# Kernel optimization log

Measured on AMD Instinct MI355X. Metric: run time of the kernel, lower is better.

## Reference

```python
import jax, jax.numpy as jnp
import numpy as np

N_HEADS = 16
D_EMB = 1024
D_HEAD = D_EMB // N_HEADS


def setup_inputs() -> dict:
    key = jax.random.key(0)
    ks = jax.random.split(key, 5)
    scale = 1.0 / np.sqrt(D_EMB)
    x = jax.random.normal(ks[0], (4, 2048, D_EMB), dtype=jnp.float32)
    W_in = jax.random.normal(ks[1], (3 * D_EMB, D_EMB), dtype=jnp.float32) * scale
    b_in = jax.random.normal(ks[2], (3 * D_EMB,), dtype=jnp.float32) * 0.01
    W_out = jax.random.normal(ks[3], (D_EMB, D_EMB), dtype=jnp.float32) * scale
    b_out = jax.random.normal(ks[4], (D_EMB,), dtype=jnp.float32) * 0.01
    return {"x": x, "W_in": W_in, "b_in": b_in, "W_out": W_out, "b_out": b_out}


def reference(x, W_in, b_in, W_out, b_out):
    b, s, d = x.shape
    qkv = x @ W_in.T + b_in  # [b, s, 3d]
    q, k, v = jnp.split(qkv, 3, axis=-1)
    def heads(t):
        return t.reshape(b, s, N_HEADS, D_HEAD).transpose(0, 2, 1, 3)  # [b,h,s,dh]
    q, k, v = heads(q), heads(k), heads(v)
    scores = jnp.einsum('bhqd,bhkd->bhqk', q, k)
    causal = jnp.tril(jnp.ones((s, s), dtype=bool))  # keep lower-triangular incl diag
    scores = jnp.where(causal, scores, -jnp.inf)
    scores = scores / np.sqrt(D_HEAD).astype(np.float32)
    w = jax.nn.softmax(scores, axis=-1)
    out = jnp.einsum('bhqk,bhkd->bhqd', w, v)  # [b,h,s,dh]
    out = out.transpose(0, 2, 1, 3).reshape(b, s, d)
    return out @ W_out.T + b_out
```

## Files before the change

kernel.cpp:

```cpp
#include <hip/hip_runtime.h>
#include <hip/hip_bf16.h>
#include <cstdint>


typedef float  floatx4  __attribute__((ext_vector_type(4)));
typedef __bf16 bf16x8   __attribute__((ext_vector_type(8)));
typedef __bf16 bf16x4   __attribute__((ext_vector_type(4)));
typedef short  shortx4  __attribute__((ext_vector_type(4)));
typedef unsigned int   uint32x2 __attribute__((ext_vector_type(2)));
typedef unsigned short ushortx8 __attribute__((ext_vector_type(8)));

#define MFMA16(a,b,c) __builtin_amdgcn_mfma_f32_16x16x32_bf16(a, b, c, 0, 0, 0)

__device__ __forceinline__ floatx4 mfma_k16(bf16x4 a, bf16x4 b, floatx4 c) {
#if defined(__HIP_DEVICE_COMPILE__)
#if __has_builtin(__builtin_amdgcn_mfma_f32_16x16x16_bf16)
  return __builtin_amdgcn_mfma_f32_16x16x16_bf16(a, b, c, 0, 0, 0);
#elif __has_builtin(__builtin_amdgcn_mfma_f32_16x16x16bf16_1k)
  return __builtin_amdgcn_mfma_f32_16x16x16bf16_1k(
      __builtin_bit_cast(shortx4, a), __builtin_bit_cast(shortx4, b), c, 0, 0, 0);
#else
  floatx4 d;
  asm("v_mfma_f32_16x16x16_bf16 %0, %1, %2, %3"
      : "=v"(d)
      : "v"(__builtin_bit_cast(uint32x2, a)),
        "v"(__builtin_bit_cast(uint32x2, b)), "v"(c));
  return d;
#endif
#else
  (void)a; (void)b;
  return c;
#endif
}

#define C_SCALE 0.18033688011112042f
#define M_STATIC 16.0f

__device__ __forceinline__ void gload_lds16(const void* g, void* l) {
  __builtin_amdgcn_global_load_lds(
      (__attribute__((address_space(1))) void*)(g),
      (__attribute__((address_space(3))) void*)(l), 16, 0, 0);
}

#define N_X4    2097152
#define N_WIN4  786432
#define N_WOUT4 262144
#define N_B4    768
__global__ __launch_bounds__(256) void cast_fused(
    const float* __restrict__ x, const float* __restrict__ W_in,
    const float* __restrict__ W_out, const float* __restrict__ b_in,
    __bf16* __restrict__ xb, __bf16* __restrict__ Winb,
    __bf16* __restrict__ Woutb, float* __restrict__ bins) {
  int i = blockIdx.x * 256 + threadIdx.x;
  if (i < N_X4) {
    const float4 v = ((const float4*)x)[i];
    bf16x4 o;
    o.x = (__bf16)v.x; o.y = (__bf16)v.y; o.z = (__bf16)v.z; o.w = (__bf16)v.w;
    ((bf16x4*)xb)[i] = o;
  } else if (i < N_X4 + N_WIN4) {
    const int j = i - N_X4;
    const float s = (j < 262144) ? C_SCALE : 1.0f;
    const float4 v = ((const float4*)W_in)[j];
    bf16x4 o;
    o.x = (__bf16)(v.x * s); o.y = (__bf16)(v.y * s);
    o.z = (__bf16)(v.z * s); o.w = (__bf16)(v.w * s);
    ((bf16x4*)Winb)[j] = o;
  } else if (i < N_X4 + N_WIN4 + N_WOUT4) {
    const int j = i - N_X4 - N_WIN4;
    const float4 v = ((const float4*)W_out)[j];
    bf16x4 o;
    o.x = (__bf16)v.x; o.y = (__bf16)v.y; o.z = (__bf16)v.z; o.w = (__bf16)v.w;
    ((bf16x4*)Woutb)[j] = o;
  } else {
    const int j = i - N_X4 - N_WIN4 - N_WOUT4;
    const float s = (j < 256) ? C_SCALE : 1.0f;
    float4 v = ((const float4*)b_in)[j];
    v.x *= s; v.y *= s; v.z *= s; v.w *= s;
    ((float4*)bins)[j] = v;
  }
}

template <int MODE>
__global__ __launch_bounds__(256) void gemm_bt(
    const __bf16* __restrict__ A, const __bf16* __restrict__ B,
    const float* __restrict__ bias, void* __restrict__ Cout,
    __bf16* __restrict__ Vt, int M, int N, int K) {
  __shared__ __bf16 As[128 * 32];
  __shared__ __bf16 Bs[128 * 32];
  const int tid = threadIdx.x;
  const int wave = tid >> 6, lane = tid & 63;
  const int quad = lane >> 4, l15 = lane & 15;
  const int wm = (wave & 1) * 64, wn = (wave >> 1) * 64;
  const long row0 = (long)blockIdx.y * 128;
  const long col0 = (long)blockIdx.x * 128;

  floatx4 acc[4][4] = {};

  const int sr = wave * 16 + (lane >> 2);
  const int sc = (lane & 3) * 8;
  const __bf16* ga = A + (row0 + sr) * (long)K + sc;
  const __bf16* gb = B + (col0 + sr) * (long)K + sc;
  __bf16* lA = As + wave * 512 + lane * 8;
  __bf16* lB = Bs + wave * 512 + lane * 8;

  for (int k0 = 0; k0 < K; k0 += 32) {
    gload_lds16(ga,                lA);
    gload_lds16(ga + 64 * (long)K, lA + 2048);
    gload_lds16(gb,                lB);
    gload_lds16(gb + 64 * (long)K, lB + 2048);
    ga += 32; gb += 32;
    __syncthreads();

    bf16x8 af[4], bfr[4];
#pragma unroll
    for (int i = 0; i < 4; ++i)
      af[i] = *(const bf16x8*)(As + (wm + i * 16 + l15) * 32 + quad * 8);
#pragma unroll
    for (int j = 0; j < 4; ++j)
      bfr[j] = *(const bf16x8*)(Bs + (wn + j * 16 + l15) * 32 + quad * 8);
#pragma unroll
    for (int i = 0; i < 4; ++i)
#pragma unroll
      for (int j = 0; j < 4; ++j)
        acc[i][j] = MFMA16(af[i], bfr[j], acc[i][j]);
    __syncthreads();
  }

#pragma unroll
  for (int i = 0; i < 4; ++i) {
    const long r0 = row0 + wm + i * 16 + quad * 4;
#pragma unroll
    for (int j = 0; j < 4; ++j) {
      const long c = col0 + wn + j * 16 + l15;
      const float bv = bias[c];
      if (MODE == 0) {
#pragma unroll
        for (int reg = 0; reg < 4; ++reg)
          ((float*)Cout)[(r0 + reg) * (long)N + c] = acc[i][j][reg] + bv;
      } else {
        if (c < 2048) {
#pragma unroll
          for (int reg = 0; reg < 4; ++reg)
            ((__bf16*)Cout)[(r0 + reg) * (long)N + c] =
                (__bf16)(acc[i][j][reg] + bv);
        } else {
          const int cc = (int)c - 2048;
          const int hh = cc >> 6, dh = cc & 63;
          const int bb = (int)(r0 >> 11), s = (int)(r0 & 2047);
          bf16x4 pk;
#pragma unroll
          for (int reg = 0; reg < 4; ++reg)
            pk[reg] = (__bf16)(acc[i][j][reg] + bv);
          *(bf16x4*)(Vt + ((long)(bb * 16 + hh) * 64 + dh) * 2048 + s) = pk;
        }
      }
    }
  }
}

__global__ __launch_bounds__(256, 4) void flash_attn(
    const __bf16* __restrict__ qkv,
    const __bf16* __restrict__ Vt,
    __bf16* __restrict__ Out) {
  constexpr int S = 2048;
  const int h = blockIdx.y, b = blockIdx.z;
  const int x = (int)(blockIdx.x + 5 * blockIdx.z + 3 * blockIdx.y) & 15;
  const int qtA = x, qtB = 31 - x;
  const int kmaxA = qtA + 1;
  const int kmax  = qtB + 1;

  __shared__ __bf16 Ks[2][64 * 72];
  __shared__ __bf16 Vs[2][64 * 72];

  const int tid = threadIdx.x, wave = tid >> 6, lane = tid & 63;
  const int quad = lane >> 4, l15 = lane & 15;

  bf16x8 qf[2][2];
  {
    const long qrA = (long)(b * S + qtA * 64 + wave * 16 + l15) * 3072 + h * 64;
    const long qrB = (long)(b * S + qtB * 64 + wave * 16 + l15) * 3072 + h * 64;
    qf[0][0] = *(const bf16x8*)(qkv + qrA + quad * 8);
    qf[0][1] = *(const bf16x8*)(qkv + qrA + 32 + quad * 8);
    qf[1][0] = *(const bf16x8*)(qkv + qrB + quad * 8);
    qf[1][1] = *(const bf16x8*)(qkv + qrB + 32 + quad * 8);
  }

  floatx4 oA[4] = {}, oB[4] = {};
  float lAcc[2] = {0.f, 0.f};

  const int srow = tid >> 3;
  const int sc8 = (tid & 7) * 8;
  const __bf16* ka = qkv + ((long)(b * S) + srow) * 3072 + 1024 + h * 64 + sc8;
  const __bf16* va = Vt + ((long)(b * 16 + h) * 64 + srow) * S + sc8;
  const int sl = srow * 72 + sc8;

  ushortx8 kr0 = *(const ushortx8*)ka;
  ushortx8 kr1 = *(const ushortx8*)(ka + 32 * 3072);
  ushortx8 vr0 = *(const ushortx8*)va;
  ushortx8 vr1 = *(const ushortx8*)(va + 32 * (long)S);
  *(ushortx8*)(&Ks[0][sl]) = kr0;
  *(ushortx8*)(&Ks[0][sl + 32 * 72]) = kr1;
  *(ushortx8*)(&Vs[0][sl]) = vr0;
  *(ushortx8*)(&Vs[0][sl + 32 * 72]) = vr1;
  kr0 = *(const ushortx8*)(ka + 64 * 3072);
  kr1 = *(const ushortx8*)(ka + 96 * 3072);
  vr0 = *(const ushortx8*)(va + 64);
  vr1 = *(const ushortx8*)(va + 32 * (long)S + 64);
  __syncthreads();

  for (int kt = 0; kt < kmax; ++kt) {
    const int cur = kt & 1;
    if (kt + 1 < kmax) {
      *(ushortx8*)(&Ks[cur ^ 1][sl]) = kr0;
      *(ushortx8*)(&Ks[cur ^ 1][sl + 32 * 72]) = kr1;
      *(ushortx8*)(&Vs[cur ^ 1][sl]) = vr0;
      *(ushortx8*)(&Vs[cur ^ 1][sl + 32 * 72]) = vr1;
    }
    if (kt + 2 < kmax) {
      const long ko = (long)(kt + 2) * 64 * 3072;
      kr0 = *(const ushortx8*)(ka + ko);
      kr1 = *(const ushortx8*)(ka + ko + 32 * 3072);
      vr0 = *(const ushortx8*)(va + (kt + 2) * 64);
      vr1 = *(const ushortx8*)(va + 32 * (long)S + (kt + 2) * 64);
    }

    const bool actA = (kt < kmaxA);
    const bool partA = (kt == qtA);
    const bool partB = (kt == qtB);

    floatx4 svA[4], svB[4];
#pragma unroll
    for (int nb = 0; nb < 4; ++nb) {
      const bf16x8 k0 = *(const bf16x8*)(&Ks[cur][(nb * 16 + l15) * 72 + quad * 8]);
      const bf16x8 k1 = *(const bf16x8*)(&Ks[cur][(nb * 16 + l15) * 72 + 32 + quad * 8]);
      if (actA) {
        floatx4 z = {0.f, 0.f, 0.f, 0.f};
        z = MFMA16(k0, qf[0][0], z);
        z = MFMA16(k1, qf[0][1], z);
        svA[nb] = z;
      }
      {
        floatx4 z = {0.f, 0.f, 0.f, 0.f};
        z = MFMA16(k0, qf[1][0], z);
        z = MFMA16(k1, qf[1][1], z);
        svB[nb] = z;
      }
    }

    if (partA) {
      const int qg = qtA * 64 + wave * 16 + l15;
#pragma unroll
      for (int nb = 0; nb < 4; ++nb) {
        const int key0 = kt * 64 + nb * 16 + quad * 4;
#pragma unroll
        for (int r = 0; r < 4; ++r)
          if (key0 + r > qg) svA[nb][r] = -1.0e30f;
      }
    }
    if (partB) {
      const int qg = qtB * 64 + wave * 16 + l15;
#pragma unroll
      for (int nb = 0; nb < 4; ++nb) {
        const int key0 = kt * 64 + nb * 16 + quad * 4;
#pragma unroll
        for (int r = 0; r < 4; ++r)
          if (key0 + r > qg) svB[nb][r] = -1.0e30f;
      }
    }

    bf16x4 pfA[4], pfB[4];
    if (actA) {
      float ls = 0.f;
#pragma unroll
      for (int nb = 0; nb < 4; ++nb)
#pragma unroll
        for (int r = 0; r < 4; ++r) {
          const float p = exp2f(svA[nb][r] - M_STATIC);
          ls += p;
          pfA[nb][r] = (__bf16)p;
        }
      ls += __shfl_xor(ls, 16, 64);
      ls += __shfl_xor(ls, 32, 64);
      lAcc[0] += ls;
    }
    {
      float ls = 0.f;
#pragma unroll
      for (int nb = 0; nb < 4; ++nb)
#pragma unroll
        for (int r = 0; r < 4; ++r) {
          const float p = exp2f(svB[nb][r] - M_STATIC);
          ls += p;
          pfB[nb][r] = (__bf16)p;
        }
      ls += __shfl_xor(ls, 16, 64);
      ls += __shfl_xor(ls, 32, 64);
      lAcc[1] += ls;
    }

#pragma unroll
    for (int mb = 0; mb < 4; ++mb) {
#pragma unroll
      for (int c = 0; c < 4; ++c) {
        const bf16x4 vf = *(const bf16x4*)(&Vs[cur][(mb * 16 + l15) * 72 + c * 16 + quad * 4]);
        if (actA) oA[mb] = mfma_k16(vf, pfA[c], oA[mb]);
        oB[mb] = mfma_k16(vf, pfB[c], oB[mb]);
      }
    }
    __syncthreads();
  }

  {
    const float inv = 1.f / lAcc[0];
    const long row = (long)(b * S + qtA * 64 + wave * 16 + l15);
#pragma unroll
    for (int mb = 0; mb < 4; ++mb) {
      bf16x4 pk;
#pragma unroll
      for (int r = 0; r < 4; ++r) pk[r] = (__bf16)(oA[mb][r] * inv);
      *(bf16x4*)(Out + row * 1024 + h * 64 + mb * 16 + quad * 4) = pk;
    }
  }
  {
    const float inv = 1.f / lAcc[1];
    const long row = (long)(b * S + qtB * 64 + wave * 16 + l15);
#pragma unroll
    for (int mb = 0; mb < 4; ++mb) {
      bf16x4 pk;
#pragma unroll
      for (int r = 0; r < 4; ++r) pk[r] = (__bf16)(oB[mb][r] * inv);
      *(bf16x4*)(Out + row * 1024 + h * 64 + mb * 16 + quad * 4) = pk;
    }
  }
}

extern "C" void kernel_launch(void* const* d_in, const int* in_sizes, int n_in,
                              void* d_out, int out_size, void* d_ws, size_t ws_size,
                              hipStream_t stream) {
  const float* x     = (const float*)d_in[0];
  const float* W_in  = (const float*)d_in[1];
  const float* b_in  = (const float*)d_in[2];
  const float* W_out = (const float*)d_in[3];
  const float* b_out = (const float*)d_in[4];

  const int BS = 4 * 2048;
  const int D = 1024, N3 = 3072;

  char* w = (char*)d_ws;
  __bf16* xb    = (__bf16*)w;  w += (size_t)BS * D * 2;
  __bf16* Winb  = (__bf16*)w;  w += (size_t)N3 * D * 2;
  __bf16* Woutb = (__bf16*)w;  w += (size_t)D * D * 2;
  __bf16* qkvb  = (__bf16*)w;  w += (size_t)BS * N3 * 2;
  __bf16* Vtb   = (__bf16*)w;  w += (size_t)64 * 64 * 2048 * 2;
  __bf16* attnb = (__bf16*)w;  w += (size_t)BS * D * 2;
  float*  bins  = (float*)w;   w += (size_t)N3 * 4;

  const int castN = N_X4 + N_WIN4 + N_WOUT4 + N_B4;
  cast_fused<<<dim3(castN / 256), 256, 0, stream>>>(
      x, W_in, W_out, b_in, xb, Winb, Woutb, bins);

  gemm_bt<2><<<dim3(N3 / 128, BS / 128), 256, 0, stream>>>(
      xb, Winb, bins, (void*)qkvb, Vtb, BS, N3, D);

  flash_attn<<<dim3(16, 16, 4), 256, 0, stream>>>(qkvb, Vtb, attnb);

  gemm_bt<0><<<dim3(D / 128, BS / 128), 256, 0, stream>>>(
      attnb, Woutb, b_out, d_out, nullptr, BS, D, D);
}
```

Before: 290.1 us.

## Load V fragments directly from global and compute row sums via MFMA

Removes the shared-memory staging of the transposed V tile. Each lane now reads its V MFMA fragments straight from global memory, with a one-step software prefetch across the mb loop. The softmax row-sum is computed by an MFMA against a ones vector instead of per-lane adds plus cross-lane shuffles. This cuts LDS traffic, LDS footprint and shuffles. In exchange it issues small uncoalesced 8-byte global loads with exposed latency, and the sum is taken from the bf16-rounded probabilities.

```diff
diff --git a/kernel.cpp b/kernel.cpp
--- a/kernel.cpp
+++ b/kernel.cpp
@@ -170,7 +170,6 @@
   const int kmax  = qtB + 1;
 
   __shared__ __bf16 Ks[2][64 * 72];
-  __shared__ __bf16 Vs[2][64 * 72];
 
   const int tid = threadIdx.x, wave = tid >> 6, lane = tid & 63;
   const int quad = lane >> 4, l15 = lane & 15;
@@ -185,27 +184,26 @@
     qf[1][1] = *(const bf16x8*)(qkv + qrB + 32 + quad * 8);
   }
 
+  bf16x4 ones4;
+#pragma unroll
+  for (int j = 0; j < 4; ++j) ones4[j] = (__bf16)1.0f;
+
   floatx4 oA[4] = {}, oB[4] = {};
-  float lAcc[2] = {0.f, 0.f};
+  floatx4 lA = {0.f, 0.f, 0.f, 0.f}, lB = {0.f, 0.f, 0.f, 0.f};
 
   const int srow = tid >> 3;
   const int sc8 = (tid & 7) * 8;
   const __bf16* ka = qkv + ((long)(b * S) + srow) * 3072 + 1024 + h * 64 + sc8;
-  const __bf16* va = Vt + ((long)(b * 16 + h) * 64 + srow) * S + sc8;
   const int sl = srow * 72 + sc8;
+
+  const __bf16* vrow = Vt + ((long)(b * 16 + h) * 64 + l15) * S + quad * 4;
 
   ushortx8 kr0 = *(const ushortx8*)ka;
   ushortx8 kr1 = *(const ushortx8*)(ka + 32 * 3072);
-  ushortx8 vr0 = *(const ushortx8*)va;
-  ushortx8 vr1 = *(const ushortx8*)(va + 32 * (long)S);
   *(ushortx8*)(&Ks[0][sl]) = kr0;
   *(ushortx8*)(&Ks[0][sl + 32 * 72]) = kr1;
-  *(ushortx8*)(&Vs[0][sl]) = vr0;
-  *(ushortx8*)(&Vs[0][sl + 32 * 72]) = vr1;
   kr0 = *(const ushortx8*)(ka + 64 * 3072);
   kr1 = *(const ushortx8*)(ka + 96 * 3072);
-  vr0 = *(const ushortx8*)(va + 64);
-  vr1 = *(const ushortx8*)(va + 32 * (long)S + 64);
   __syncthreads();
 
   for (int kt = 0; kt < kmax; ++kt) {
@@ -213,20 +211,21 @@
     if (kt + 1 < kmax) {
       *(ushortx8*)(&Ks[cur ^ 1][sl]) = kr0;
       *(ushortx8*)(&Ks[cur ^ 1][sl + 32 * 72]) = kr1;
-      *(ushortx8*)(&Vs[cur ^ 1][sl]) = vr0;
-      *(ushortx8*)(&Vs[cur ^ 1][sl + 32 * 72]) = vr1;
     }
     if (kt + 2 < kmax) {
       const long ko = (long)(kt + 2) * 64 * 3072;
       kr0 = *(const ushortx8*)(ka + ko);
       kr1 = *(const ushortx8*)(ka + ko + 32 * 3072);
-      vr0 = *(const ushortx8*)(va + (kt + 2) * 64);
-      vr1 = *(const ushortx8*)(va + 32 * (long)S + (kt + 2) * 64);
     }
 
     const bool actA = (kt < kmaxA);
     const bool partA = (kt == qtA);
     const bool partB = (kt == qtB);
+    const __bf16* vkt = vrow + kt * 64;
+
+    bf16x4 vf[4];
+#pragma unroll
+    for (int c = 0; c < 4; ++c) vf[c] = *(const bf16x4*)(vkt + c * 16);
 
     floatx4 svA[4], svB[4];
 #pragma unroll
@@ -270,48 +269,45 @@
 
     bf16x4 pfA[4], pfB[4];
     if (actA) {
-      float ls = 0.f;
 #pragma unroll
       for (int nb = 0; nb < 4; ++nb)
 #pragma unroll
-        for (int r = 0; r < 4; ++r) {
-          const float p = exp2f(svA[nb][r] - M_STATIC);
-          ls += p;
-          pfA[nb][r] = (__bf16)p;
-        }
-      ls += __shfl_xor(ls, 16, 64);
-      ls += __shfl_xor(ls, 32, 64);
-      lAcc[0] += ls;
+        for (int r = 0; r < 4; ++r)
+          pfA[nb][r] = (__bf16)exp2f(svA[nb][r] - M_STATIC);
+#pragma unroll
+      for (int c = 0; c < 4; ++c) lA = mfma_k16(ones4, pfA[c], lA);
     }
     {
-      float ls = 0.f;
 #pragma unroll
       for (int nb = 0; nb < 4; ++nb)
 #pragma unroll
-        for (int r = 0; r < 4; ++r) {
-          const float p = exp2f(svB[nb][r] - M_STATIC);
-          ls += p;
-          pfB[nb][r] = (__bf16)p;
-        }
-      ls += __shfl_xor(ls, 16, 64);
-      ls += __shfl_xor(ls, 32, 64);
-      lAcc[1] += ls;
+        for (int r = 0; r < 4; ++r)
+          pfB[nb][r] = (__bf16)exp2f(svB[nb][r] - M_STATIC);
+#pragma unroll
+      for (int c = 0; c < 4; ++c) lB = mfma_k16(ones4, pfB[c], lB);
     }
 
 #pragma unroll
     for (int mb = 0; mb < 4; ++mb) {
+      bf16x4 vfn[4];
+      if (mb < 3) {
+#pragma unroll
+        for (int c = 0; c < 4; ++c)
+          vfn[c] = *(const bf16x4*)(vkt + (mb + 1) * 16 * (long)S + c * 16);
+      }
 #pragma unroll
       for (int c = 0; c < 4; ++c) {
-        const bf16x4 vf = *(const bf16x4*)(&Vs[cur][(mb * 16 + l15) * 72 + c * 16 + quad * 4]);
-        if (actA) oA[mb] = mfma_k16(vf, pfA[c], oA[mb]);
-        oB[mb] = mfma_k16(vf, pfB[c], oB[mb]);
-      }
+        if (actA) oA[mb] = mfma_k16(vf[c], pfA[c], oA[mb]);
+        oB[mb] = mfma_k16(vf[c], pfB[c], oB[mb]);
+      }
+#pragma unroll
+      for (int c = 0; c < 4; ++c) vf[c] = vfn[c];
     }
     __syncthreads();
   }
 
   {
-    const float inv = 1.f / lAcc[0];
+    const float inv = 1.f / lA[0];
     const long row = (long)(b * S + qtA * 64 + wave * 16 + l15);
 #pragma unroll
     for (int mb = 0; mb < 4; ++mb) {
@@ -322,7 +318,7 @@
     }
   }
   {
-    const float inv = 1.f / lAcc[1];
+    const float inv = 1.f / lB[0];
     const long row = (long)(b * S + qtB * 64 + wave * 16 + l15);
 #pragma unroll
     for (int mb = 0; mb < 4; ++mb) {
```

Result: slower. 455.6 us (+57.1%).
